# Kernel tuning notes

Measured on AMD Instinct MI355X. Metric: run time of the kernel, lower is better.

Reference implementation:

```python
import jax, jax.numpy as jnp
import numpy as np

EPS = 1e-7  # tf.keras.backend.epsilon()
ROUTING = 3
C, L = 32, 32

def squash(s):
    # 'Dynamic routing between capsules' squash: (|s|^2/(1+|s|^2)) * s/|s|
    n = jnp.linalg.norm(s, axis=-1, keepdims=True)
    return (n ** 2 / (1 + n ** 2) / (n + EPS)) * s

def setup_inputs() -> dict:
    key = jax.random.key(0)
    k1, k2 = jax.random.split(key)
    B, H, Wd, iC, iL = 32, 8, 8, 32, 32
    inputs = jax.random.normal(k1, (B, H, Wd, iC, iL), dtype=jnp.float32)
    N = H * Wd * iC  # 2048 input capsules
    # glorot_uniform for W: [N, input_L, C*L]
    limit = float(np.sqrt(6.0 / (iL + C * L)))
    W = jax.random.uniform(k2, (N, iL, C * L), minval=-limit, maxval=limit, dtype=jnp.float32)
    biases = jnp.zeros((C, L), dtype=jnp.float32)  # 'zeros' initializer
    return {"inputs": inputs, "W": W, "biases": biases}

def reference(inputs, W, biases):
    B = inputs.shape[0]
    N, iL = W.shape[0], W.shape[1]
    x = inputs.reshape(B, N, iL)
    # per-capsule prediction: u[b,j,k] = sum_i x[b,j,i] * W[j,i,k]
    u = jnp.einsum('bji,jik->bjk', x, W).reshape(B, N, C, L)
    b = jnp.zeros((B, N, C, 1), dtype=u.dtype)
    v = jnp.zeros((B, C, L), dtype=u.dtype)
    for r in range(ROUTING):
        c = jax.nn.softmax(b, axis=2)                 # coupling coeffs over C
        s = jnp.sum(u * c, axis=1) + biases           # [B,C,L]
        # NOTE: CapsuleAttentionBlock applied here in original (source not
        # provided in this module); treated as identity.
        v = squash(s)                                 # [B,C,L]
        if r < ROUTING - 1:
            b = b + jnp.sum(u * v[:, None, :, :], axis=-1, keepdims=True)
    return v
```

## Files before the change

kernel.cpp:

```cpp
#include <hip/hip_runtime.h>
#include <hip/hip_bf16.h>

#define NB    32
#define NCAP  2048
#define CL    1024
#define ILEN  32

__device__ inline unsigned short f32_to_bf16_rne(float f) {
    unsigned int u = __float_as_uint(f);
    u += 0x7FFFu + ((u >> 16) & 1u);
    return (unsigned short)(u >> 16);
}

__device__ inline void unpack8(uint4 a, float* f) {
    f[0] = __uint_as_float(a.x << 16);
    f[1] = __uint_as_float(a.x & 0xFFFF0000u);
    f[2] = __uint_as_float(a.y << 16);
    f[3] = __uint_as_float(a.y & 0xFFFF0000u);
    f[4] = __uint_as_float(a.z << 16);
    f[5] = __uint_as_float(a.z & 0xFFFF0000u);
    f[6] = __uint_as_float(a.w << 16);
    f[7] = __uint_as_float(a.w & 0xFFFF0000u);
}

__global__ __launch_bounds__(256) void compute_u(const float* __restrict__ x,
                                                 const float* __restrict__ W,
                                                 unsigned short* __restrict__ u) {
    const int j  = blockIdx.x >> 2;
    const int kq = blockIdx.x & 3;
    const int t  = threadIdx.x;

    __shared__ float wl[32 * 256];
    __shared__ float xs[32 * 32];

    const float* Wj = W + (size_t)j * (ILEN * CL) + kq * 256;
#pragma unroll
    for (int it = 0; it < 8; ++it) {
        int f   = t + it * 256;
        int i   = f >> 6;
        int col = (f & 63) << 2;
        *(float4*)(wl + i * 256 + col) = *(const float4*)(Wj + (size_t)i * CL + col);
    }
    {
        int b  = t >> 3;
        int i4 = (t & 7) << 2;
        float4 v = *(const float4*)(x + ((size_t)b * NCAP + j) * ILEN + i4);
        xs[(i4 + 0) * 32 + b] = v.x;
        xs[(i4 + 1) * 32 + b] = v.y;
        xs[(i4 + 2) * 32 + b] = v.z;
        xs[(i4 + 3) * 32 + b] = v.w;
    }
    __syncthreads();

    const int lane = t & 63;
    const int wv   = t >> 6;

    float acc[8][4];
#pragma unroll
    for (int bb = 0; bb < 8; ++bb)
#pragma unroll
        for (int q = 0; q < 4; ++q) acc[bb][q] = 0.f;

#pragma unroll 4
    for (int i = 0; i < 32; ++i) {
        float4 w4 = *(const float4*)(wl + i * 256 + (lane << 2));
        float4 xa = *(const float4*)(xs + i * 32 + wv * 8);
        float4 xb = *(const float4*)(xs + i * 32 + wv * 8 + 4);
        float xv[8] = {xa.x, xa.y, xa.z, xa.w, xb.x, xb.y, xb.z, xb.w};
#pragma unroll
        for (int bb = 0; bb < 8; ++bb) {
            acc[bb][0] += xv[bb] * w4.x;
            acc[bb][1] += xv[bb] * w4.y;
            acc[bb][2] += xv[bb] * w4.z;
            acc[bb][3] += xv[bb] * w4.w;
        }
    }

    const int k = kq * 256 + (lane << 2);
#pragma unroll
    for (int bb = 0; bb < 8; ++bb) {
        int b = wv * 8 + bb;
        ushort4 o;
        o.x = f32_to_bf16_rne(acc[bb][0]);
        o.y = f32_to_bf16_rne(acc[bb][1]);
        o.z = f32_to_bf16_rne(acc[bb][2]);
        o.w = f32_to_bf16_rne(acc[bb][3]);
        *(ushort4*)(u + ((size_t)b * NCAP + j) * CL + k) = o;
    }
}

template<bool HAS_V>
__global__ __launch_bounds__(256) void route_pass(const unsigned short* __restrict__ u,
                                                  const float* __restrict__ vlog,
                                                  float* __restrict__ spart) {
    const int b    = blockIdx.x;
    const int jc   = blockIdx.y;
    const int t    = threadIdx.x;
    const int wv   = t >> 6;
    const int lane = t & 63;
    const int c0   = lane >> 2;
    const int sub  = lane & 3;
    const int e0   = c0 * 32 + sub * 8;

    float vme0[8], vme1[8];
    if (HAS_V) {
        const float* vb = vlog + b * CL;
        *(float4*)(vme0)     = *(const float4*)(vb + e0);
        *(float4*)(vme0 + 4) = *(const float4*)(vb + e0 + 4);
        *(float4*)(vme1)     = *(const float4*)(vb + e0 + 512);
        *(float4*)(vme1 + 4) = *(const float4*)(vb + e0 + 516);
    }

    const int jbase = jc * 128 + wv * 32;
    const unsigned short* ub = u + ((size_t)b * NCAP + jbase) * CL;

    float acc0[8], acc1[8];
#pragma unroll
    for (int e = 0; e < 8; ++e) { acc0[e] = 0.f; acc1[e] = 0.f; }

    uint4 a0 = *(const uint4*)(ub + 0 * CL + e0);
    uint4 g0 = *(const uint4*)(ub + 0 * CL + e0 + 512);
    uint4 a1 = *(const uint4*)(ub + 1 * CL + e0);
    uint4 g1 = *(const uint4*)(ub + 1 * CL + e0 + 512);

    for (int jj = 0; jj < 32; ++jj) {
        int jn = (jj + 2 < 32) ? (jj + 2) : 31;
        uint4 a2 = *(const uint4*)(ub + (size_t)jn * CL + e0);
        uint4 g2 = *(const uint4*)(ub + (size_t)jn * CL + e0 + 512);

        float uf0[8], uf1[8];
        unpack8(a0, uf0);
        unpack8(g0, uf1);

        float cw0, cw1;
        if (HAS_V) {
            float p0 = 0.f, p1 = 0.f;
#pragma unroll
            for (int e = 0; e < 8; ++e) { p0 += uf0[e] * vme0[e]; p1 += uf1[e] * vme1[e]; }
            p0 += __shfl_xor(p0, 1); p0 += __shfl_xor(p0, 2);
            p1 += __shfl_xor(p1, 1); p1 += __shfl_xor(p1, 2);
            float m = fmaxf(p0, p1);
            m = fmaxf(m, __shfl_xor(m, 4));
            m = fmaxf(m, __shfl_xor(m, 8));
            m = fmaxf(m, __shfl_xor(m, 16));
            m = fmaxf(m, __shfl_xor(m, 32));
            float ex0 = __expf(p0 - m);
            float ex1 = __expf(p1 - m);
            float ssum = ex0 + ex1;
            ssum += __shfl_xor(ssum, 4);
            ssum += __shfl_xor(ssum, 8);
            ssum += __shfl_xor(ssum, 16);
            ssum += __shfl_xor(ssum, 32);
            float inv = __builtin_amdgcn_rcpf(ssum);
            cw0 = ex0 * inv;
            cw1 = ex1 * inv;
        } else {
            cw0 = 0.03125f;
            cw1 = 0.03125f;
        }
#pragma unroll
        for (int e = 0; e < 8; ++e) {
            acc0[e] += cw0 * uf0[e];
            acc1[e] += cw1 * uf1[e];
        }
        a0 = a1; g0 = g1; a1 = a2; g1 = g2;
    }

    __shared__ float red[4][1024];
    *(float4*)(&red[wv][e0])       = *(float4*)(acc0);
    *(float4*)(&red[wv][e0 + 4])   = *(float4*)(acc0 + 4);
    *(float4*)(&red[wv][e0 + 512]) = *(float4*)(acc1);
    *(float4*)(&red[wv][e0 + 516]) = *(float4*)(acc1 + 4);
    __syncthreads();

    const int o = t * 4;
    float4 r0 = *(float4*)(&red[0][o]);
    float4 r1 = *(float4*)(&red[1][o]);
    float4 r2 = *(float4*)(&red[2][o]);
    float4 r3 = *(float4*)(&red[3][o]);
    float4 r;
    r.x = (r0.x + r1.x) + (r2.x + r3.x);
    r.y = (r0.y + r1.y) + (r2.y + r3.y);
    r.z = (r0.z + r1.z) + (r2.z + r3.z);
    r.w = (r0.w + r1.w) + (r2.w + r3.w);
    *(float4*)(spart + ((size_t)b * 16 + jc) * CL + o) = r;
}

__global__ __launch_bounds__(256) void squash_kernel(const float* __restrict__ spart,
                                                     const float* __restrict__ biases,
                                                     float* __restrict__ vout,
                                                     float* __restrict__ vlog_out,
                                                     const float* __restrict__ vprev) {
    const int b = blockIdx.x;
    const int t = threadIdx.x;

    float4 sv = make_float4(0.f, 0.f, 0.f, 0.f);
#pragma unroll
    for (int p = 0; p < 16; ++p) {
        float4 q = *(const float4*)(spart + ((size_t)b * 16 + p) * CL + t * 4);
        sv.x += q.x; sv.y += q.y; sv.z += q.z; sv.w += q.w;
    }
    float4 bi = *(const float4*)(biases + t * 4);
    sv.x += bi.x; sv.y += bi.y; sv.z += bi.z; sv.w += bi.w;

    float n2 = sv.x * sv.x + sv.y * sv.y + sv.z * sv.z + sv.w * sv.w;
    n2 += __shfl_xor(n2, 1);
    n2 += __shfl_xor(n2, 2);
    n2 += __shfl_xor(n2, 4);

    float n = sqrtf(n2);
    float f = n2 / ((1.f + n2) * (n + 1e-7f));

    float4 v;
    v.x = f * sv.x; v.y = f * sv.y; v.z = f * sv.z; v.w = f * sv.w;
    *(float4*)(vout + b * CL + t * 4) = v;

    if (vlog_out != nullptr) {
        float4 a = make_float4(0.f, 0.f, 0.f, 0.f);
        if (vprev != nullptr) a = *(const float4*)(vprev + b * CL + t * 4);
        float4 o;
        o.x = v.x + a.x; o.y = v.y + a.y; o.z = v.z + a.z; o.w = v.w + a.w;
        *(float4*)(vlog_out + b * CL + t * 4) = o;
    }
}

extern "C" void kernel_launch(void* const* d_in, const int* in_sizes, int n_in,
                              void* d_out, int out_size, void* d_ws, size_t ws_size,
                              hipStream_t stream) {
    const float* x      = (const float*)d_in[0];
    const float* W      = (const float*)d_in[1];
    const float* biases = (const float*)d_in[2];
    float* out = (float*)d_out;

    unsigned short* u = (unsigned short*)d_ws;
    float* fb    = (float*)((char*)d_ws + (size_t)NB * NCAP * CL * 2);
    float* spart = fb;
    float* v0    = spart + 524288;
    float* vl2   = v0 + 32768;
    float* vdmp  = vl2 + 32768;

    compute_u<<<NCAP * 4, 256, 0, stream>>>(x, W, u);

    dim3 rg(NB, 16);
    route_pass<false><<<rg, 256, 0, stream>>>(u, nullptr, spart);
    squash_kernel<<<NB, 256, 0, stream>>>(spart, biases, v0, nullptr, nullptr);
    route_pass<true><<<rg, 256, 0, stream>>>(u, v0, spart);
    squash_kernel<<<NB, 256, 0, stream>>>(spart, biases, vdmp, vl2, v0);
    route_pass<true><<<rg, 256, 0, stream>>>(u, vl2, spart);
    squash_kernel<<<NB, 256, 0, stream>>>(spart, biases, out, nullptr, nullptr);
}
```

Baseline: 461.4 us.

## Widen compute_u register tile and process two capsules per routing iteration

compute_u now has each thread compute an 8x8 batch-by-output tile and read W straight from global memory instead of staging it in LDS, which halves the block count and doubles per-thread reuse. The route pass handles two input capsules per loop iteration with a deeper prefetch window, interleaving two independent softmax shuffle chains to hide latency. The cost is more registers per thread, which may lower occupancy, and W loads in compute_u that no longer go through shared memory.

```diff
diff --git a/kernel.cpp b/kernel.cpp
--- a/kernel.cpp
+++ b/kernel.cpp
@@ -6,10 +6,12 @@
 #define CL    1024
 #define ILEN  32
 
-__device__ inline unsigned short f32_to_bf16_rne(float f) {
-    unsigned int u = __float_as_uint(f);
-    u += 0x7FFFu + ((u >> 16) & 1u);
-    return (unsigned short)(u >> 16);
+__device__ inline unsigned int pack2_bf16(float lo, float hi) {
+    unsigned int a = __float_as_uint(lo);
+    a += 0x7FFFu + ((a >> 16) & 1u);
+    unsigned int b = __float_as_uint(hi);
+    b += 0x7FFFu + ((b >> 16) & 1u);
+    return (a >> 16) | (b & 0xFFFF0000u);
 }
 
 __device__ inline void unpack8(uint4 a, float* f) {
@@ -26,66 +28,58 @@
 __global__ __launch_bounds__(256) void compute_u(const float* __restrict__ x,
                                                  const float* __restrict__ W,
                                                  unsigned short* __restrict__ u) {
-    const int j  = blockIdx.x >> 2;
-    const int kq = blockIdx.x & 3;
-    const int t  = threadIdx.x;
-
-    __shared__ float wl[32 * 256];
-    __shared__ float xs[32 * 32];
-
-    const float* Wj = W + (size_t)j * (ILEN * CL) + kq * 256;
-#pragma unroll
-    for (int it = 0; it < 8; ++it) {
-        int f   = t + it * 256;
-        int i   = f >> 6;
-        int col = (f & 63) << 2;
-        *(float4*)(wl + i * 256 + col) = *(const float4*)(Wj + (size_t)i * CL + col);
-    }
+    const int j    = blockIdx.x >> 1;
+    const int kh   = blockIdx.x & 1;
+    const int t    = threadIdx.x;
+    const int wv   = t >> 6;
+    const int lane = t & 63;
+
+    __shared__ float xs[32][32];
+
     {
-        int b  = t >> 3;
-        int i4 = (t & 7) << 2;
+        int b  = t & 31;
+        int i4 = (t >> 5) << 2;
         float4 v = *(const float4*)(x + ((size_t)b * NCAP + j) * ILEN + i4);
-        xs[(i4 + 0) * 32 + b] = v.x;
-        xs[(i4 + 1) * 32 + b] = v.y;
-        xs[(i4 + 2) * 32 + b] = v.z;
-        xs[(i4 + 3) * 32 + b] = v.w;
+        xs[i4 + 0][b] = v.x;
+        xs[i4 + 1][b] = v.y;
+        xs[i4 + 2][b] = v.z;
+        xs[i4 + 3][b] = v.w;
     }
     __syncthreads();
 
-    const int lane = t & 63;
-    const int wv   = t >> 6;
-
-    float acc[8][4];
+    const float* Wb = W + (size_t)j * (ILEN * CL) + kh * 512 + lane * 8;
+
+    float acc[8][8];
 #pragma unroll
     for (int bb = 0; bb < 8; ++bb)
 #pragma unroll
-        for (int q = 0; q < 4; ++q) acc[bb][q] = 0.f;
+        for (int kk = 0; kk < 8; ++kk) acc[bb][kk] = 0.f;
 
 #pragma unroll 4
     for (int i = 0; i < 32; ++i) {
-        float4 w4 = *(const float4*)(wl + i * 256 + (lane << 2));
-        float4 xa = *(const float4*)(xs + i * 32 + wv * 8);
-        float4 xb = *(const float4*)(xs + i * 32 + wv * 8 + 4);
-        float xv[8] = {xa.x, xa.y, xa.z, xa.w, xb.x, xb.y, xb.z, xb.w};
-#pragma unroll
-        for (int bb = 0; bb < 8; ++bb) {
-            acc[bb][0] += xv[bb] * w4.x;
-            acc[bb][1] += xv[bb] * w4.y;
-            acc[bb][2] += xv[bb] * w4.z;
-            acc[bb][3] += xv[bb] * w4.w;
-        }
-    }
-
-    const int k = kq * 256 + (lane << 2);
+        float4 w0 = *(const float4*)(Wb + (size_t)i * CL);
+        float4 w1 = *(const float4*)(Wb + (size_t)i * CL + 4);
+        float4 x0 = *(const float4*)(&xs[i][wv * 8]);
+        float4 x1 = *(const float4*)(&xs[i][wv * 8 + 4]);
+        float wk[8] = {w0.x, w0.y, w0.z, w0.w, w1.x, w1.y, w1.z, w1.w};
+        float xv[8] = {x0.x, x0.y, x0.z, x0.w, x1.x, x1.y, x1.z, x1.w};
+#pragma unroll
+        for (int bb = 0; bb < 8; ++bb)
+#pragma unroll
+            for (int kk = 0; kk < 8; ++kk)
+                acc[bb][kk] += xv[bb] * wk[kk];
+    }
+
+    const int k = kh * 512 + lane * 8;
 #pragma unroll
     for (int bb = 0; bb < 8; ++bb) {
         int b = wv * 8 + bb;
-        ushort4 o;
-        o.x = f32_to_bf16_rne(acc[bb][0]);
-        o.y = f32_to_bf16_rne(acc[bb][1]);
-        o.z = f32_to_bf16_rne(acc[bb][2]);
-        o.w = f32_to_bf16_rne(acc[bb][3]);
-        *(ushort4*)(u + ((size_t)b * NCAP + j) * CL + k) = o;
+        uint4 o;
+        o.x = pack2_bf16(acc[bb][0], acc[bb][1]);
+        o.y = pack2_bf16(acc[bb][2], acc[bb][3]);
+        o.z = pack2_bf16(acc[bb][4], acc[bb][5]);
+        o.w = pack2_bf16(acc[bb][6], acc[bb][7]);
+        *(uint4*)(u + ((size_t)b * NCAP + j) * CL + k) = o;
     }
 }
 
@@ -112,58 +106,82 @@
     }
 
     const int jbase = jc * 128 + wv * 32;
-    const unsigned short* ub = u + ((size_t)b * NCAP + jbase) * CL;
+    const unsigned short* up = u + ((size_t)b * NCAP + jbase) * CL + e0;
 
     float acc0[8], acc1[8];
 #pragma unroll
     for (int e = 0; e < 8; ++e) { acc0[e] = 0.f; acc1[e] = 0.f; }
 
-    uint4 a0 = *(const uint4*)(ub + 0 * CL + e0);
-    uint4 g0 = *(const uint4*)(ub + 0 * CL + e0 + 512);
-    uint4 a1 = *(const uint4*)(ub + 1 * CL + e0);
-    uint4 g1 = *(const uint4*)(ub + 1 * CL + e0 + 512);
-
-    for (int jj = 0; jj < 32; ++jj) {
-        int jn = (jj + 2 < 32) ? (jj + 2) : 31;
-        uint4 a2 = *(const uint4*)(ub + (size_t)jn * CL + e0);
-        uint4 g2 = *(const uint4*)(ub + (size_t)jn * CL + e0 + 512);
-
-        float uf0[8], uf1[8];
-        unpack8(a0, uf0);
-        unpack8(g0, uf1);
-
-        float cw0, cw1;
+    uint4 ca0 = *(const uint4*)(up + 0 * CL);
+    uint4 cg0 = *(const uint4*)(up + 0 * CL + 512);
+    uint4 ca1 = *(const uint4*)(up + 1 * CL);
+    uint4 cg1 = *(const uint4*)(up + 1 * CL + 512);
+    uint4 pa0 = *(const uint4*)(up + 2 * CL);
+    uint4 pg0 = *(const uint4*)(up + 2 * CL + 512);
+    uint4 pa1 = *(const uint4*)(up + 3 * CL);
+    uint4 pg1 = *(const uint4*)(up + 3 * CL + 512);
+
+    for (int jj = 0; jj < 32; jj += 2) {
+        const int j4 = (jj + 4 < 32) ? jj + 4 : 31;
+        const int j5 = (jj + 5 < 32) ? jj + 5 : 31;
+        uint4 na0 = *(const uint4*)(up + (size_t)j4 * CL);
+        uint4 ng0 = *(const uint4*)(up + (size_t)j4 * CL + 512);
+        uint4 na1 = *(const uint4*)(up + (size_t)j5 * CL);
+        uint4 ng1 = *(const uint4*)(up + (size_t)j5 * CL + 512);
+
+        float uf0[8], uf1[8], uf2[8], uf3[8];
+        unpack8(ca0, uf0); unpack8(cg0, uf1);
+        unpack8(ca1, uf2); unpack8(cg1, uf3);
+
+        float cw0, cw1, cw2, cw3;
         if (HAS_V) {
-            float p0 = 0.f, p1 = 0.f;
-#pragma unroll
-            for (int e = 0; e < 8; ++e) { p0 += uf0[e] * vme0[e]; p1 += uf1[e] * vme1[e]; }
+            float p0 = 0.f, p1 = 0.f, p2 = 0.f, p3 = 0.f;
+#pragma unroll
+            for (int e = 0; e < 8; ++e) {
+                p0 += uf0[e] * vme0[e];
+                p1 += uf1[e] * vme1[e];
+                p2 += uf2[e] * vme0[e];
+                p3 += uf3[e] * vme1[e];
+            }
             p0 += __shfl_xor(p0, 1); p0 += __shfl_xor(p0, 2);
             p1 += __shfl_xor(p1, 1); p1 += __shfl_xor(p1, 2);
-            float m = fmaxf(p0, p1);
-            m = fmaxf(m, __shfl_xor(m, 4));
-            m = fmaxf(m, __shfl_xor(m, 8));
-            m = fmaxf(m, __shfl_xor(m, 16));
-            m = fmaxf(m, __shfl_xor(m, 32));
-            float ex0 = __expf(p0 - m);
-            float ex1 = __expf(p1 - m);
-            float ssum = ex0 + ex1;
-            ssum += __shfl_xor(ssum, 4);
-            ssum += __shfl_xor(ssum, 8);
-            ssum += __shfl_xor(ssum, 16);
-            ssum += __shfl_xor(ssum, 32);
-            float inv = __builtin_amdgcn_rcpf(ssum);
-            cw0 = ex0 * inv;
-            cw1 = ex1 * inv;
+            p2 += __shfl_xor(p2, 1); p2 += __shfl_xor(p2, 2);
+            p3 += __shfl_xor(p3, 1); p3 += __shfl_xor(p3, 2);
+            float m0 = fmaxf(p0, p1);
+            float m1 = fmaxf(p2, p3);
+            m0 = fmaxf(m0, __shfl_xor(m0, 4));
+            m1 = fmaxf(m1, __shfl_xor(m1, 4));
+            m0 = fmaxf(m0, __shfl_xor(m0, 8));
+            m1 = fmaxf(m1, __shfl_xor(m1, 8));
+            m0 = fmaxf(m0, __shfl_xor(m0, 16));
+            m1 = fmaxf(m1, __shfl_xor(m1, 16));
+            m0 = fmaxf(m0, __shfl_xor(m0, 32));
+            m1 = fmaxf(m1, __shfl_xor(m1, 32));
+            float e00 = __expf(p0 - m0), e01 = __expf(p1 - m0);
+            float e10 = __expf(p2 - m1), e11 = __expf(p3 - m1);
+            float s0 = e00 + e01, s1 = e10 + e11;
+            s0 += __shfl_xor(s0, 4);
+            s1 += __shfl_xor(s1, 4);
+            s0 += __shfl_xor(s0, 8);
+            s1 += __shfl_xor(s1, 8);
+            s0 += __shfl_xor(s0, 16);
+            s1 += __shfl_xor(s1, 16);
+            s0 += __shfl_xor(s0, 32);
+            s1 += __shfl_xor(s1, 32);
+            float i0 = __builtin_amdgcn_rcpf(s0);
+            float i1 = __builtin_amdgcn_rcpf(s1);
+            cw0 = e00 * i0; cw1 = e01 * i0;
+            cw2 = e10 * i1; cw3 = e11 * i1;
         } else {
-            cw0 = 0.03125f;
-            cw1 = 0.03125f;
+            cw0 = cw1 = cw2 = cw3 = 0.03125f;
         }
 #pragma unroll
         for (int e = 0; e < 8; ++e) {
-            acc0[e] += cw0 * uf0[e];
-            acc1[e] += cw1 * uf1[e];
+            acc0[e] += cw0 * uf0[e] + cw2 * uf2[e];
+            acc1[e] += cw1 * uf1[e] + cw3 * uf3[e];
         }
-        a0 = a1; g0 = g1; a1 = a2; g1 = g2;
+        ca0 = pa0; cg0 = pg0; ca1 = pa1; cg1 = pg1;
+        pa0 = na0; pg0 = ng0; pa1 = na1; pg1 = ng1;
     }
 
     __shared__ float red[4][1024];
@@ -239,7 +257,7 @@
     float* vl2   = v0 + 32768;
     float* vdmp  = vl2 + 32768;
 
-    compute_u<<<NCAP * 4, 256, 0, stream>>>(x, W, u);
+    compute_u<<<NCAP * 2, 256, 0, stream>>>(x, W, u);
 
     dim3 rg(NB, 16);
     route_pass<false><<<rg, 256, 0, stream>>>(u, nullptr, spart);
```

Result: slower. 479.1 us (+3.8%).
